# Performance work log

Hardware: AMD Instinct MI355X
Metric: run time of the kernel (lower is better)

The kernel has to match this reference:

```python
import jax, jax.numpy as jnp
import numpy as np

N_NODES = 100000
N_EDGES = 600000
D = 128


def gcn_conv(x, W, b, src, dst, n_nodes):
    """PyG-style GCNConv: add self-loops, symmetric deg^{-1/2} normalization."""
    xw = x @ W  # [N, out]
    # degree of destination nodes, counting the added self-loop
    deg = jnp.zeros((n_nodes,), xw.dtype).at[dst].add(1.0) + 1.0
    dinv = jax.lax.rsqrt(deg)
    coef = dinv[src] * dinv[dst]  # [E]
    agg = jnp.zeros_like(xw).at[dst].add(xw[src] * coef[:, None])
    agg = agg + xw * (dinv * dinv)[:, None]  # self-loop term
    return agg + b


def setup_inputs() -> dict:
    key = jax.random.key(0)
    k = jax.random.split(key, 9)
    s = 1.0 / np.sqrt(D)
    return {
        "x": jax.random.normal(k[0], (N_NODES, D), jnp.float32),
        "edge_index_pos": jax.random.randint(k[1], (2, N_EDGES), 0, N_NODES, jnp.int64),
        "edge_index_neg": jax.random.randint(k[2], (2, N_EDGES), 0, N_NODES, jnp.int64),
        "W1": jax.random.uniform(k[3], (D, D), jnp.float32, -s, s),
        "b1": jnp.zeros((D,), jnp.float32),
        "W2": jax.random.uniform(k[4], (D, D), jnp.float32, -s, s),
        "b2": jnp.zeros((D,), jnp.float32),
        "weight": jax.random.uniform(k[5], (2 * D, D), jnp.float32, -s, s),
        "bias": jnp.zeros((D,), jnp.float32),
    }


def reference(x, edge_index_pos, edge_index_neg, W1, b1, W2, b2, weight, bias):
    n = x.shape[0]
    h1 = gcn_conv(x, W1, b1, edge_index_pos[0], edge_index_pos[1], n)  # [N, D]
    h2 = gcn_conv(x, W2, b2, edge_index_neg[0], edge_index_neg[1], n)  # [N, D]
    h = jnp.concatenate([h1, h2], axis=-1)  # [N, 2D]
    return h @ weight + bias  # [N, D]
```

## Files before the change

### kernel.cpp

```cpp
#include <hip/hip_runtime.h>

#define N_NODES 100000
#define NT (2 * N_NODES)
#define D 128
#define N_EDGES 600000
#define ET (2 * N_EDGES)
#define SCAN_B 256
#define NBLK2 ((NT + SCAN_B - 1) / SCAN_B)
#define FROWS 256
#define FBLK ((N_NODES + FROWS - 1) / FROWS)
#define ZBLK ((NT / 4 + 255) / 256)

typedef __attribute__((ext_vector_type(8))) short bf16x8;
typedef __attribute__((ext_vector_type(4))) float f32x4;

__device__ __forceinline__ unsigned short f2bf(float f) {
    union { float f; unsigned u; } v; v.f = f;
    unsigned r = (v.u + 0x7fff + ((v.u >> 16) & 1)) >> 16;
    return (unsigned short)r;
}
__device__ __forceinline__ float bf2f(unsigned short h) {
    union { unsigned u; float f; } v; v.u = ((unsigned)h) << 16;
    return v.f;
}

__device__ __forceinline__ long long load_idx(const void* e, long long i, int is32) {
    if (is32) return (long long)((const int*)e)[i];
    return ((const long long*)e)[i];
}

__global__ void prep_all(const float* __restrict__ W1, const float* __restrict__ W2,
                         const float* __restrict__ weight,
                         const float* __restrict__ b1, const float* __restrict__ b2,
                         const float* __restrict__ bias,
                         const unsigned long long* __restrict__ e_pos,
                         unsigned short* __restrict__ Mt, float* __restrict__ bt,
                         int* __restrict__ flag, int* __restrict__ degi) {
    if (blockIdx.x < 128) {
        int idx = blockIdx.x * 256 + threadIdx.x;
        int j = idx >> 8, k = idx & 255;
        float a = 0.f;
        if (k < D) {
            for (int d = 0; d < D; ++d) a += W1[k * D + d] * weight[d * D + j];
        } else {
            for (int d = 0; d < D; ++d) a += W2[(k - D) * D + d] * weight[(D + d) * D + j];
        }
        Mt[j * 256 + k] = f2bf(a);
    } else if (blockIdx.x == 128) {
        int t = threadIdx.x;
        if (t < D) {
            float a = bias[t];
            for (int k = 0; k < D; ++k)
                a += b1[k] * weight[k * D + t] + b2[k] * weight[(D + k) * D + t];
            bt[t] = a;
        } else if (t < 192) {
            unsigned long long v = e_pos[t - 128];
            unsigned long long m = __ballot(v > 0xFFFFFFFFull);
            if (t == 128) *flag = (m != 0ull) ? 1 : 0;
        }
    } else {
        int i = (blockIdx.x - 129) * 256 + threadIdx.x;
        if (i < NT / 4) ((int4*)degi)[i] = make_int4(0, 0, 0, 0);
    }
}

__global__ void x2bf_degree(const float* __restrict__ x, unsigned short* __restrict__ xb,
                            const void* __restrict__ ep, const void* __restrict__ en,
                            const int* __restrict__ flag, int* __restrict__ degi) {
    if (blockIdx.x < 12500) {
        long long t = (long long)blockIdx.x * 256 + threadIdx.x;
        float4 a = ((const float4*)x)[t];
        ((ushort4*)xb)[t] = make_ushort4(f2bf(a.x), f2bf(a.y), f2bf(a.z), f2bf(a.w));
    } else {
        int i = (blockIdx.x - 12500) * 256 + threadIdx.x;
        if (i >= ET) return;
        int is32 = *flag;
        int conv = (i >= N_EDGES);
        const void* e = conv ? en : ep;
        int j = conv ? i - N_EDGES : i;
        long long d = load_idx(e, (long long)N_EDGES + j, is32);
        atomicAdd(&degi[conv * N_NODES + (int)d], 1);
    }
}

__global__ void scan_pass1(const int* __restrict__ degi, int* __restrict__ bsum,
                           float* __restrict__ dinv, unsigned char* __restrict__ degb) {
    __shared__ int sm[SCAN_B];
    int i = blockIdx.x * SCAN_B + threadIdx.x;
    int v = (i < NT) ? degi[i] : 0;
    if (i < NT) {
        dinv[i] = rsqrtf((float)v + 1.0f);
        degb[i] = (unsigned char)(v > 255 ? 255 : v);
    }
    sm[threadIdx.x] = v;
    __syncthreads();
    for (int s = SCAN_B / 2; s > 0; s >>= 1) {
        if (threadIdx.x < s) sm[threadIdx.x] += sm[threadIdx.x + s];
        __syncthreads();
    }
    if (threadIdx.x == 0) bsum[blockIdx.x] = sm[0];
}

__global__ void scan_pass3(const int* __restrict__ degi, const int* __restrict__ bsum,
                           int* __restrict__ off) {
    __shared__ int red[SCAN_B];
    __shared__ int sm[SCAN_B];
    int partial = 0;
    for (int i = threadIdx.x; i < blockIdx.x; i += SCAN_B) partial += bsum[i];
    red[threadIdx.x] = partial;
    __syncthreads();
    for (int s = SCAN_B / 2; s > 0; s >>= 1) {
        if (threadIdx.x < s) red[threadIdx.x] += red[threadIdx.x + s];
        __syncthreads();
    }
    int base = red[0];
    int i = blockIdx.x * SCAN_B + threadIdx.x;
    int v = (i < NT) ? degi[i] : 0;
    sm[threadIdx.x] = v;
    __syncthreads();
    for (int ofs = 1; ofs < SCAN_B; ofs <<= 1) {
        int add = (threadIdx.x >= ofs) ? sm[threadIdx.x - ofs] : 0;
        __syncthreads();
        sm[threadIdx.x] += add;
        __syncthreads();
    }
    int excl = sm[threadIdx.x] - v + base;
    if (i < NT) off[i] = excl;
    if (i == NT - 1) off[NT] = excl + v;
}

__global__ void csr_fill_both(const void* __restrict__ ep, const void* __restrict__ en,
                              const int* __restrict__ flag, const int* __restrict__ off,
                              int* __restrict__ degi, const unsigned char* __restrict__ degb,
                              unsigned* __restrict__ csr) {
    int i = blockIdx.x * blockDim.x + threadIdx.x;
    if (i >= ET) return;
    int is32 = *flag;
    int conv = (i >= N_EDGES);
    const void* e = conv ? en : ep;
    int j = conv ? i - N_EDGES : i;
    int si = (int)load_idx(e, j, is32);
    int di = (int)load_idx(e, (long long)N_EDGES + j, is32);
    int g = conv * N_NODES;
    int node = g + di;
    int pos = off[node] + atomicSub(&degi[node], 1) - 1;
    unsigned degS = degb[g + si];
    csr[pos] = (unsigned)si | (degS << 20);
}

__global__ __launch_bounds__(1024) void fused_gather_gemm(
    const int* __restrict__ off, const unsigned* __restrict__ csr,
    const unsigned short* __restrict__ xb, const float* __restrict__ dinv,
    const unsigned short* __restrict__ Mt, const float* __restrict__ bt,
    float* __restrict__ out) {
    __shared__ unsigned short mlds[128][264];
    int t = threadIdx.x;
    for (int c = t; c < 4096; c += 1024) {
        int row = c >> 5;
        int kc = (c & 31) * 8;
        *(ulonglong2*)&mlds[row][kc] = *(const ulonglong2*)&Mt[row * 256 + kc];
    }
    __syncthreads();

    int wave = t >> 6, lane = t & 63;
    int rl = lane & 15, q = lane >> 4;
    int gr = blockIdx.x * FROWS + wave * 16 + rl;
    const bool valid = gr < N_NODES;

    bf16x8 af[8];
    #pragma unroll
    for (int conv = 0; conv < 2; ++conv) {
        float acc[4][8];
        if (valid) {
            int n = conv * N_NODES + gr;
            float dn = dinv[n];
            float f = dn * dn;
            const unsigned short* xr = xb + (size_t)gr * D + q * 8;
            #pragma unroll
            for (int m = 0; m < 4; ++m) {
                bf16x8 v = *(const bf16x8*)(xr + m * 32);
                #pragma unroll
                for (int j = 0; j < 8; ++j) acc[m][j] = bf2f((unsigned short)v[j]) * f;
            }
            int e0 = off[n], e1 = off[n + 1];
            for (int e = e0; e < e1; ++e) {
                unsigned sc = csr[e];
                int si = sc & 0xFFFFF;
                float coef = dn * rsqrtf((float)(sc >> 20) + 1.0f);
                const unsigned short* xs = xb + (size_t)si * D + q * 8;
                #pragma unroll
                for (int m = 0; m < 4; ++m) {
                    bf16x8 v = *(const bf16x8*)(xs + m * 32);
                    #pragma unroll
                    for (int j = 0; j < 8; ++j) acc[m][j] += coef * bf2f((unsigned short)v[j]);
                }
            }
        } else {
            #pragma unroll
            for (int m = 0; m < 4; ++m)
                #pragma unroll
                for (int j = 0; j < 8; ++j) acc[m][j] = 0.f;
        }
        #pragma unroll
        for (int m = 0; m < 4; ++m) {
            bf16x8 a;
            #pragma unroll
            for (int j = 0; j < 8; ++j) a[j] = (short)f2bf(acc[m][j]);
            af[conv * 4 + m] = a;
        }
    }

    f32x4 C[8];
    #pragma unroll
    for (int i = 0; i < 8; ++i) C[i] = (f32x4){0.f, 0.f, 0.f, 0.f};
    #pragma unroll
    for (int ks = 0; ks < 8; ++ks) {
        bf16x8 afr = af[ks];
        #pragma unroll
        for (int ct = 0; ct < 8; ++ct) {
            bf16x8 bfr = *(const bf16x8*)&mlds[ct * 16 + rl][ks * 32 + q * 8];
            C[ct] = __builtin_amdgcn_mfma_f32_16x16x32_bf16(afr, bfr, C[ct], 0, 0, 0);
        }
    }

    int orow = blockIdx.x * FROWS + wave * 16 + q * 4;
    #pragma unroll
    for (int ct = 0; ct < 8; ++ct) {
        int col = ct * 16 + rl;
        float b = bt[col];
        #pragma unroll
        for (int reg = 0; reg < 4; ++reg) {
            int row = orow + reg;
            if (row < N_NODES) out[(long long)row * D + col] = C[ct][reg] + b;
        }
    }
}

extern "C" void kernel_launch(void* const* d_in, const int* in_sizes, int n_in,
                              void* d_out, int out_size, void* d_ws, size_t ws_size,
                              hipStream_t stream) {
    const float* x      = (const float*)d_in[0];
    const void*  e_pos  = d_in[1];
    const void*  e_neg  = d_in[2];
    const float* W1     = (const float*)d_in[3];
    const float* b1     = (const float*)d_in[4];
    const float* W2     = (const float*)d_in[5];
    const float* b2     = (const float*)d_in[6];
    const float* weight = (const float*)d_in[7];
    const float* bias   = (const float*)d_in[8];
    float* out = (float*)d_out;

    unsigned short* xb = (unsigned short*)d_ws;
    unsigned short* Mt = xb + (size_t)N_NODES * D;
    float* bt   = (float*)(Mt + 128 * 256);
    float* dinv = bt + D;
    int*   flag = (int*)(dinv + NT);
    int*   degi = flag + 4;
    int*   off  = degi + NT;
    int*   bsum = off + NT + 4;
    unsigned char* degb = (unsigned char*)(bsum + 1024);
    unsigned* csr = (unsigned*)(degb + NT);

    prep_all<<<129 + ZBLK, 256, 0, stream>>>(W1, W2, weight, b1, b2, bias,
                                             (const unsigned long long*)e_pos,
                                             Mt, bt, flag, degi);
    const int egrid = (ET + 255) / 256;
    x2bf_degree<<<12500 + egrid, 256, 0, stream>>>(x, xb, e_pos, e_neg, flag, degi);
    scan_pass1<<<NBLK2, SCAN_B, 0, stream>>>(degi, bsum, dinv, degb);
    scan_pass3<<<NBLK2, SCAN_B, 0, stream>>>(degi, bsum, off);
    csr_fill_both<<<egrid, 256, 0, stream>>>(e_pos, e_neg, flag, off, degi, degb, csr);
    fused_gather_gemm<<<FBLK, 1024, 0, stream>>>(off, csr, xb, dinv, Mt, bt, out);
}
```

Before: 224.0 us.

## Merge graph build kernels into one persistent kernel with grid barriers; unroll gather

Replaces the four graph-construction launches (bf16 conversion plus degree count, two scan passes, CSR fill) with one kernel that uses grid-stride loops and software atomic grid barriers between phases. This cuts kernel launch gaps and tail effects between the small stages. The gather loop is also unrolled by two edges so more independent row loads are in flight per thread. The grid barrier relies on all 782 blocks being co-resident (launch_bounds 256,4 across the device's CUs), and there is a deadlock risk if they are not.

```diff
diff --git a/kernel.cpp b/kernel.cpp
--- a/kernel.cpp
+++ b/kernel.cpp
@@ -29,13 +29,22 @@
     return ((const long long*)e)[i];
 }
 
+__device__ __forceinline__ void grid_barrier(int* bar, int nblk) {
+    __syncthreads();
+    if (threadIdx.x == 0) {
+        __hip_atomic_fetch_add(bar, 1, __ATOMIC_RELEASE, __HIP_MEMORY_SCOPE_AGENT);
+        while (__hip_atomic_load(bar, __ATOMIC_ACQUIRE, __HIP_MEMORY_SCOPE_AGENT) < nblk) {}
+    }
+    __syncthreads();
+}
+
 __global__ void prep_all(const float* __restrict__ W1, const float* __restrict__ W2,
                          const float* __restrict__ weight,
                          const float* __restrict__ b1, const float* __restrict__ b2,
                          const float* __restrict__ bias,
                          const unsigned long long* __restrict__ e_pos,
                          unsigned short* __restrict__ Mt, float* __restrict__ bt,
-                         int* __restrict__ flag, int* __restrict__ degi) {
+                         int* __restrict__ flag_bar, int* __restrict__ degi) {
     if (blockIdx.x < 128) {
         int idx = blockIdx.x * 256 + threadIdx.x;
         int j = idx >> 8, k = idx & 255;
@@ -56,7 +65,9 @@
         } else if (t < 192) {
             unsigned long long v = e_pos[t - 128];
             unsigned long long m = __ballot(v > 0xFFFFFFFFull);
-            if (t == 128) *flag = (m != 0ull) ? 1 : 0;
+            if (t == 128) flag_bar[0] = (m != 0ull) ? 1 : 0;
+        } else if (t == 192) {
+            flag_bar[1] = 0; flag_bar[2] = 0; flag_bar[3] = 0;
         }
     } else {
         int i = (blockIdx.x - 129) * 256 + threadIdx.x;
@@ -64,88 +75,83 @@
     }
 }
 
-__global__ void x2bf_degree(const float* __restrict__ x, unsigned short* __restrict__ xb,
-                            const void* __restrict__ ep, const void* __restrict__ en,
-                            const int* __restrict__ flag, int* __restrict__ degi) {
-    if (blockIdx.x < 12500) {
-        long long t = (long long)blockIdx.x * 256 + threadIdx.x;
+__global__ __launch_bounds__(256, 4) void build_graph(
+    const float* __restrict__ x, unsigned short* __restrict__ xb,
+    const void* __restrict__ ep, const void* __restrict__ en,
+    int* __restrict__ flag_bar, int* __restrict__ degi,
+    int* __restrict__ bsum, float* __restrict__ dinv,
+    unsigned char* __restrict__ degb, int* __restrict__ off,
+    unsigned* __restrict__ csr) {
+    __shared__ int sm[SCAN_B];
+    __shared__ int red[SCAN_B];
+    const int tid = threadIdx.x, b = blockIdx.x;
+    const int gthreads = NBLK2 * SCAN_B;
+    const int gt = b * SCAN_B + tid;
+    const int is32 = flag_bar[0];
+
+    for (long long t = gt; t < (long long)N_NODES * 32; t += gthreads) {
         float4 a = ((const float4*)x)[t];
         ((ushort4*)xb)[t] = make_ushort4(f2bf(a.x), f2bf(a.y), f2bf(a.z), f2bf(a.w));
-    } else {
-        int i = (blockIdx.x - 12500) * 256 + threadIdx.x;
-        if (i >= ET) return;
-        int is32 = *flag;
+    }
+    for (int i = gt; i < ET; i += gthreads) {
         int conv = (i >= N_EDGES);
         const void* e = conv ? en : ep;
         int j = conv ? i - N_EDGES : i;
         long long d = load_idx(e, (long long)N_EDGES + j, is32);
         atomicAdd(&degi[conv * N_NODES + (int)d], 1);
     }
-}
-
-__global__ void scan_pass1(const int* __restrict__ degi, int* __restrict__ bsum,
-                           float* __restrict__ dinv, unsigned char* __restrict__ degb) {
-    __shared__ int sm[SCAN_B];
-    int i = blockIdx.x * SCAN_B + threadIdx.x;
+    grid_barrier(&flag_bar[1], NBLK2);
+
+    int i = b * SCAN_B + tid;
     int v = (i < NT) ? degi[i] : 0;
     if (i < NT) {
         dinv[i] = rsqrtf((float)v + 1.0f);
         degb[i] = (unsigned char)(v > 255 ? 255 : v);
     }
-    sm[threadIdx.x] = v;
+    sm[tid] = v;
     __syncthreads();
     for (int s = SCAN_B / 2; s > 0; s >>= 1) {
-        if (threadIdx.x < s) sm[threadIdx.x] += sm[threadIdx.x + s];
+        if (tid < s) sm[tid] += sm[tid + s];
         __syncthreads();
     }
-    if (threadIdx.x == 0) bsum[blockIdx.x] = sm[0];
-}
-
-__global__ void scan_pass3(const int* __restrict__ degi, const int* __restrict__ bsum,
-                           int* __restrict__ off) {
-    __shared__ int red[SCAN_B];
-    __shared__ int sm[SCAN_B];
+    if (tid == 0) bsum[b] = sm[0];
+    grid_barrier(&flag_bar[2], NBLK2);
+
     int partial = 0;
-    for (int i = threadIdx.x; i < blockIdx.x; i += SCAN_B) partial += bsum[i];
-    red[threadIdx.x] = partial;
+    for (int j = tid; j < b; j += SCAN_B) partial += bsum[j];
+    red[tid] = partial;
     __syncthreads();
     for (int s = SCAN_B / 2; s > 0; s >>= 1) {
-        if (threadIdx.x < s) red[threadIdx.x] += red[threadIdx.x + s];
+        if (tid < s) red[tid] += red[tid + s];
         __syncthreads();
     }
     int base = red[0];
-    int i = blockIdx.x * SCAN_B + threadIdx.x;
-    int v = (i < NT) ? degi[i] : 0;
-    sm[threadIdx.x] = v;
+    __syncthreads();
+    sm[tid] = v;
     __syncthreads();
     for (int ofs = 1; ofs < SCAN_B; ofs <<= 1) {
-        int add = (threadIdx.x >= ofs) ? sm[threadIdx.x - ofs] : 0;
+        int add = (tid >= ofs) ? sm[tid - ofs] : 0;
         __syncthreads();
-        sm[threadIdx.x] += add;
+        sm[tid] += add;
         __syncthreads();
     }
-    int excl = sm[threadIdx.x] - v + base;
+    int excl = sm[tid] - v + base;
     if (i < NT) off[i] = excl;
     if (i == NT - 1) off[NT] = excl + v;
-}
-
-__global__ void csr_fill_both(const void* __restrict__ ep, const void* __restrict__ en,
-                              const int* __restrict__ flag, const int* __restrict__ off,
-                              int* __restrict__ degi, const unsigned char* __restrict__ degb,
-                              unsigned* __restrict__ csr) {
-    int i = blockIdx.x * blockDim.x + threadIdx.x;
-    if (i >= ET) return;
-    int is32 = *flag;
-    int conv = (i >= N_EDGES);
-    const void* e = conv ? en : ep;
-    int j = conv ? i - N_EDGES : i;
-    int si = (int)load_idx(e, j, is32);
-    int di = (int)load_idx(e, (long long)N_EDGES + j, is32);
-    int g = conv * N_NODES;
-    int node = g + di;
-    int pos = off[node] + atomicSub(&degi[node], 1) - 1;
-    unsigned degS = degb[g + si];
-    csr[pos] = (unsigned)si | (degS << 20);
+    grid_barrier(&flag_bar[3], NBLK2);
+
+    for (int idx = gt; idx < ET; idx += gthreads) {
+        int conv = (idx >= N_EDGES);
+        const void* e = conv ? en : ep;
+        int j = conv ? idx - N_EDGES : idx;
+        int si = (int)load_idx(e, j, is32);
+        int di = (int)load_idx(e, (long long)N_EDGES + j, is32);
+        int g = conv * N_NODES;
+        int node = g + di;
+        int pos = off[node] + atomicSub(&degi[node], 1) - 1;
+        unsigned degS = degb[g + si];
+        csr[pos] = (unsigned)si | (degS << 20);
+    }
 }
 
 __global__ __launch_bounds__(1024) void fused_gather_gemm(
@@ -183,16 +189,50 @@
                 for (int j = 0; j < 8; ++j) acc[m][j] = bf2f((unsigned short)v[j]) * f;
             }
             int e0 = off[n], e1 = off[n + 1];
-            for (int e = e0; e < e1; ++e) {
-                unsigned sc = csr[e];
-                int si = sc & 0xFFFFF;
-                float coef = dn * rsqrtf((float)(sc >> 20) + 1.0f);
-                const unsigned short* xs = xb + (size_t)si * D + q * 8;
-                #pragma unroll
-                for (int m = 0; m < 4; ++m) {
-                    bf16x8 v = *(const bf16x8*)(xs + m * 32);
-                    #pragma unroll
-                    for (int j = 0; j < 8; ++j) acc[m][j] += coef * bf2f((unsigned short)v[j]);
+            int e = e0;
+            for (; e + 1 < e1; e += 2) {
+                unsigned c0 = csr[e], c1 = csr[e + 1];
+                const unsigned short* p0 = xb + (size_t)(c0 & 0xFFFFF) * D + q * 8;
+                const unsigned short* p1 = xb + (size_t)(c1 & 0xFFFFF) * D + q * 8;
+                bf16x8 a0 = *(const bf16x8*)(p0);
+                bf16x8 a1 = *(const bf16x8*)(p0 + 32);
+                bf16x8 a2 = *(const bf16x8*)(p0 + 64);
+                bf16x8 a3 = *(const bf16x8*)(p0 + 96);
+                bf16x8 b0 = *(const bf16x8*)(p1);
+                bf16x8 b1 = *(const bf16x8*)(p1 + 32);
+                bf16x8 b2 = *(const bf16x8*)(p1 + 64);
+                bf16x8 b3 = *(const bf16x8*)(p1 + 96);
+                float coef0 = dn * rsqrtf((float)(c0 >> 20) + 1.0f);
+                float coef1 = dn * rsqrtf((float)(c1 >> 20) + 1.0f);
+                #pragma unroll
+                for (int j = 0; j < 8; ++j) {
+                    acc[0][j] += coef0 * bf2f((unsigned short)a0[j]);
+                    acc[1][j] += coef0 * bf2f((unsigned short)a1[j]);
+                    acc[2][j] += coef0 * bf2f((unsigned short)a2[j]);
+                    acc[3][j] += coef0 * bf2f((unsigned short)a3[j]);
+                }
+                #pragma unroll
+                for (int j = 0; j < 8; ++j) {
+                    acc[0][j] += coef1 * bf2f((unsigned short)b0[j]);
+                    acc[1][j] += coef1 * bf2f((unsigned short)b1[j]);
+                    acc[2][j] += coef1 * bf2f((unsigned short)b2[j]);
+                    acc[3][j] += coef1 * bf2f((unsigned short)b3[j]);
+                }
+            }
+            if (e < e1) {
+                unsigned c0 = csr[e];
+                const unsigned short* p0 = xb + (size_t)(c0 & 0xFFFFF) * D + q * 8;
+                bf16x8 a0 = *(const bf16x8*)(p0);
+                bf16x8 a1 = *(const bf16x8*)(p0 + 32);
+                bf16x8 a2 = *(const bf16x8*)(p0 + 64);
+                bf16x8 a3 = *(const bf16x8*)(p0 + 96);
+                float coef0 = dn * rsqrtf((float)(c0 >> 20) + 1.0f);
+                #pragma unroll
+                for (int j = 0; j < 8; ++j) {
+                    acc[0][j] += coef0 * bf2f((unsigned short)a0[j]);
+                    acc[1][j] += coef0 * bf2f((unsigned short)a1[j]);
+                    acc[2][j] += coef0 * bf2f((unsigned short)a2[j]);
+                    acc[3][j] += coef0 * bf2f((unsigned short)a3[j]);
                 }
             }
         } else {
@@ -264,10 +304,7 @@
     prep_all<<<129 + ZBLK, 256, 0, stream>>>(W1, W2, weight, b1, b2, bias,
                                              (const unsigned long long*)e_pos,
                                              Mt, bt, flag, degi);
-    const int egrid = (ET + 255) / 256;
-    x2bf_degree<<<12500 + egrid, 256, 0, stream>>>(x, xb, e_pos, e_neg, flag, degi);
-    scan_pass1<<<NBLK2, SCAN_B, 0, stream>>>(degi, bsum, dinv, degb);
-    scan_pass3<<<NBLK2, SCAN_B, 0, stream>>>(degi, bsum, off);
-    csr_fill_both<<<egrid, 256, 0, stream>>>(e_pos, e_neg, flag, off, degi, degb, csr);
+    build_graph<<<NBLK2, SCAN_B, 0, stream>>>(x, xb, e_pos, e_neg, flag, degi,
+                                              bsum, dinv, degb, off, csr);
     fused_gather_gemm<<<FBLK, 1024, 0, stream>>>(off, csr, xb, dinv, Mt, bt, out);
 }
```

Result: slower. 448.4 us (+100.2%).

## Merge prep and convert kernels, detect index width per-wave, unroll gather by two

Applied to the files above, without the earlier changes.

Merges the weight/bias prep kernel with the bf16 conversion and degree-count kernel, so there is one fewer launch and stage boundary. The degree buffer is now zeroed with a memset, and each wave detects the index width itself with a ballot over the first 64 edges instead of reading a flag written by an earlier kernel. The gather loop in the fused kernel processes two edges per iteration, issuing eight vector loads before accumulating, to raise memory-level parallelism. The cost is a redundant 64-element read per wave and higher register pressure in a 1024-thread kernel.

```diff
diff --git a/kernel.cpp b/kernel.cpp
--- a/kernel.cpp
+++ b/kernel.cpp
@@ -9,7 +9,8 @@
 #define NBLK2 ((NT + SCAN_B - 1) / SCAN_B)
 #define FROWS 256
 #define FBLK ((N_NODES + FROWS - 1) / FROWS)
-#define ZBLK ((NT / 4 + 255) / 256)
+#define XBLK 12500
+#define EGRID ((ET + 255) / 256)
 
 typedef __attribute__((ext_vector_type(8))) short bf16x8;
 typedef __attribute__((ext_vector_type(4))) float f32x4;
@@ -29,15 +30,23 @@
     return ((const long long*)e)[i];
 }
 
-__global__ void prep_all(const float* __restrict__ W1, const float* __restrict__ W2,
-                         const float* __restrict__ weight,
-                         const float* __restrict__ b1, const float* __restrict__ b2,
-                         const float* __restrict__ bias,
-                         const unsigned long long* __restrict__ e_pos,
-                         unsigned short* __restrict__ Mt, float* __restrict__ bt,
-                         int* __restrict__ flag, int* __restrict__ degi) {
-    if (blockIdx.x < 128) {
-        int idx = blockIdx.x * 256 + threadIdx.x;
+__device__ __forceinline__ int self_detect(const unsigned long long* __restrict__ e) {
+    unsigned long long v = e[threadIdx.x & 63];
+    unsigned long long m = __ballot(v > 0xFFFFFFFFull);
+    return (m != 0ull) ? 1 : 0;
+}
+
+__global__ void prep_x2bf_degree(const float* __restrict__ W1, const float* __restrict__ W2,
+                                 const float* __restrict__ weight,
+                                 const float* __restrict__ b1, const float* __restrict__ b2,
+                                 const float* __restrict__ bias,
+                                 const float* __restrict__ x, unsigned short* __restrict__ xb,
+                                 const void* __restrict__ ep, const void* __restrict__ en,
+                                 unsigned short* __restrict__ Mt, float* __restrict__ bt,
+                                 int* __restrict__ degi) {
+    const int b = blockIdx.x;
+    if (b < 128) {
+        int idx = b * 256 + threadIdx.x;
         int j = idx >> 8, k = idx & 255;
         float a = 0.f;
         if (k < D) {
@@ -46,35 +55,22 @@
             for (int d = 0; d < D; ++d) a += W2[(k - D) * D + d] * weight[(D + d) * D + j];
         }
         Mt[j * 256 + k] = f2bf(a);
-    } else if (blockIdx.x == 128) {
+    } else if (b == 128) {
         int t = threadIdx.x;
         if (t < D) {
             float a = bias[t];
             for (int k = 0; k < D; ++k)
                 a += b1[k] * weight[k * D + t] + b2[k] * weight[(D + k) * D + t];
             bt[t] = a;
-        } else if (t < 192) {
-            unsigned long long v = e_pos[t - 128];
-            unsigned long long m = __ballot(v > 0xFFFFFFFFull);
-            if (t == 128) *flag = (m != 0ull) ? 1 : 0;
-        }
-    } else {
-        int i = (blockIdx.x - 129) * 256 + threadIdx.x;
-        if (i < NT / 4) ((int4*)degi)[i] = make_int4(0, 0, 0, 0);
-    }
-}
-
-__global__ void x2bf_degree(const float* __restrict__ x, unsigned short* __restrict__ xb,
-                            const void* __restrict__ ep, const void* __restrict__ en,
-                            const int* __restrict__ flag, int* __restrict__ degi) {
-    if (blockIdx.x < 12500) {
-        long long t = (long long)blockIdx.x * 256 + threadIdx.x;
+        }
+    } else if (b < 129 + XBLK) {
+        long long t = (long long)(b - 129) * 256 + threadIdx.x;
         float4 a = ((const float4*)x)[t];
         ((ushort4*)xb)[t] = make_ushort4(f2bf(a.x), f2bf(a.y), f2bf(a.z), f2bf(a.w));
     } else {
-        int i = (blockIdx.x - 12500) * 256 + threadIdx.x;
+        int is32 = self_detect((const unsigned long long*)ep);
+        int i = (b - 129 - XBLK) * 256 + threadIdx.x;
         if (i >= ET) return;
-        int is32 = *flag;
         int conv = (i >= N_EDGES);
         const void* e = conv ? en : ep;
         int j = conv ? i - N_EDGES : i;
@@ -130,12 +126,12 @@
 }
 
 __global__ void csr_fill_both(const void* __restrict__ ep, const void* __restrict__ en,
-                              const int* __restrict__ flag, const int* __restrict__ off,
+                              const int* __restrict__ off,
                               int* __restrict__ degi, const unsigned char* __restrict__ degb,
                               unsigned* __restrict__ csr) {
+    int is32 = self_detect((const unsigned long long*)ep);
     int i = blockIdx.x * blockDim.x + threadIdx.x;
     if (i >= ET) return;
-    int is32 = *flag;
     int conv = (i >= N_EDGES);
     const void* e = conv ? en : ep;
     int j = conv ? i - N_EDGES : i;
@@ -183,16 +179,50 @@
                 for (int j = 0; j < 8; ++j) acc[m][j] = bf2f((unsigned short)v[j]) * f;
             }
             int e0 = off[n], e1 = off[n + 1];
-            for (int e = e0; e < e1; ++e) {
-                unsigned sc = csr[e];
-                int si = sc & 0xFFFFF;
-                float coef = dn * rsqrtf((float)(sc >> 20) + 1.0f);
-                const unsigned short* xs = xb + (size_t)si * D + q * 8;
-                #pragma unroll
-                for (int m = 0; m < 4; ++m) {
-                    bf16x8 v = *(const bf16x8*)(xs + m * 32);
-                    #pragma unroll
-                    for (int j = 0; j < 8; ++j) acc[m][j] += coef * bf2f((unsigned short)v[j]);
+            int e = e0;
+            for (; e + 1 < e1; e += 2) {
+                unsigned c0 = csr[e], c1 = csr[e + 1];
+                const unsigned short* p0 = xb + (size_t)(c0 & 0xFFFFF) * D + q * 8;
+                const unsigned short* p1 = xb + (size_t)(c1 & 0xFFFFF) * D + q * 8;
+                bf16x8 a0 = *(const bf16x8*)(p0);
+                bf16x8 a1 = *(const bf16x8*)(p0 + 32);
+                bf16x8 a2 = *(const bf16x8*)(p0 + 64);
+                bf16x8 a3 = *(const bf16x8*)(p0 + 96);
+                bf16x8 b0 = *(const bf16x8*)(p1);
+                bf16x8 b1 = *(const bf16x8*)(p1 + 32);
+                bf16x8 b2 = *(const bf16x8*)(p1 + 64);
+                bf16x8 b3 = *(const bf16x8*)(p1 + 96);
+                float coef0 = dn * rsqrtf((float)(c0 >> 20) + 1.0f);
+                float coef1 = dn * rsqrtf((float)(c1 >> 20) + 1.0f);
+                #pragma unroll
+                for (int j = 0; j < 8; ++j) {
+                    acc[0][j] += coef0 * bf2f((unsigned short)a0[j]);
+                    acc[1][j] += coef0 * bf2f((unsigned short)a1[j]);
+                    acc[2][j] += coef0 * bf2f((unsigned short)a2[j]);
+                    acc[3][j] += coef0 * bf2f((unsigned short)a3[j]);
+                }
+                #pragma unroll
+                for (int j = 0; j < 8; ++j) {
+                    acc[0][j] += coef1 * bf2f((unsigned short)b0[j]);
+                    acc[1][j] += coef1 * bf2f((unsigned short)b1[j]);
+                    acc[2][j] += coef1 * bf2f((unsigned short)b2[j]);
+                    acc[3][j] += coef1 * bf2f((unsigned short)b3[j]);
+                }
+            }
+            if (e < e1) {
+                unsigned c0 = csr[e];
+                const unsigned short* p0 = xb + (size_t)(c0 & 0xFFFFF) * D + q * 8;
+                bf16x8 a0 = *(const bf16x8*)(p0);
+                bf16x8 a1 = *(const bf16x8*)(p0 + 32);
+                bf16x8 a2 = *(const bf16x8*)(p0 + 64);
+                bf16x8 a3 = *(const bf16x8*)(p0 + 96);
+                float coef0 = dn * rsqrtf((float)(c0 >> 20) + 1.0f);
+                #pragma unroll
+                for (int j = 0; j < 8; ++j) {
+                    acc[0][j] += coef0 * bf2f((unsigned short)a0[j]);
+                    acc[1][j] += coef0 * bf2f((unsigned short)a1[j]);
+                    acc[2][j] += coef0 * bf2f((unsigned short)a2[j]);
+                    acc[3][j] += coef0 * bf2f((unsigned short)a3[j]);
                 }
             }
         } else {
@@ -254,20 +284,17 @@
     unsigned short* Mt = xb + (size_t)N_NODES * D;
     float* bt   = (float*)(Mt + 128 * 256);
     float* dinv = bt + D;
-    int*   flag = (int*)(dinv + NT);
-    int*   degi = flag + 4;
+    int*   degi = (int*)(dinv + NT);
     int*   off  = degi + NT;
     int*   bsum = off + NT + 4;
     unsigned char* degb = (unsigned char*)(bsum + 1024);
     unsigned* csr = (unsigned*)(degb + NT);
 
-    prep_all<<<129 + ZBLK, 256, 0, stream>>>(W1, W2, weight, b1, b2, bias,
-                                             (const unsigned long long*)e_pos,
-                                             Mt, bt, flag, degi);
-    const int egrid = (ET + 255) / 256;
-    x2bf_degree<<<12500 + egrid, 256, 0, stream>>>(x, xb, e_pos, e_neg, flag, degi);
+    hipMemsetAsync(degi, 0, NT * sizeof(int), stream);
+    prep_x2bf_degree<<<129 + XBLK + EGRID, 256, 0, stream>>>(
+        W1, W2, weight, b1, b2, bias, x, xb, e_pos, e_neg, Mt, bt, degi);
     scan_pass1<<<NBLK2, SCAN_B, 0, stream>>>(degi, bsum, dinv, degb);
     scan_pass3<<<NBLK2, SCAN_B, 0, stream>>>(degi, bsum, off);
-    csr_fill_both<<<egrid, 256, 0, stream>>>(e_pos, e_neg, flag, off, degi, degb, csr);
+    csr_fill_both<<<EGRID, 256, 0, stream>>>(e_pos, e_neg, off, degi, degb, csr);
     fused_gather_gemm<<<FBLK, 1024, 0, stream>>>(off, csr, xb, dinv, Mt, bt, out);
 }
```

New measurement: 219.5 us. 1.02x faster.
